# Kernel optimization log

Hardware: AMD Instinct MI355X
Metric: run time of the kernel (lower is better)

Reference implementation:

```python
import jax, jax.numpy as jnp
import numpy as np

D_MODEL = 1024
NUM_HEADS = 16
D_K = D_MODEL // NUM_HEADS
B, N = 4, 2048


def setup_inputs() -> dict:
    key = jax.random.key(0)
    ks = jax.random.split(key, 5)
    scale = 1.0 / np.sqrt(D_MODEL)
    return {
        "x": jax.random.normal(ks[0], (B, N, D_MODEL), dtype=jnp.float32),
        "wq": jax.random.normal(ks[1], (D_MODEL, D_MODEL), dtype=jnp.float32) * scale,
        "wk": jax.random.normal(ks[2], (D_MODEL, D_MODEL), dtype=jnp.float32) * scale,
        "wv": jax.random.normal(ks[3], (D_MODEL, D_MODEL), dtype=jnp.float32) * scale,
        "wo": jax.random.normal(ks[4], (D_MODEL, D_MODEL), dtype=jnp.float32) * scale,
    }


def reference(x, wq, wk, wv, wo):
    b, n, d = x.shape
    # torch Linear(weight W) computes x @ W.T
    def proj(w):
        return (x @ w.T).reshape(b, n, NUM_HEADS, D_K).transpose(0, 2, 1, 3)  # [B,H,N,d_k]
    Q, K, V = proj(wq), proj(wk), proj(wv)
    scores = jnp.einsum("bhqd,bhkd->bhqk", Q, K) / jnp.sqrt(jnp.float32(D_K))
    causal = jnp.tril(jnp.ones((n, n), dtype=bool))
    scores = jnp.where(causal, scores, jnp.float32(-jnp.inf))
    attn = jax.nn.softmax(scores, axis=-1)
    vals = jnp.einsum("bhqk,bhkd->bhqd", attn, V)  # [B,H,N,d_k]
    vals = vals.transpose(0, 2, 1, 3).reshape(b, n, d)
    out = vals @ wo.T
    return (out, K, V)
```

## Files before the change

### kernel.cpp

```cpp
#include <hip/hip_runtime.h>
#include <hip/hip_bf16.h>

typedef __bf16 bf16_t;
typedef __bf16 bf16x8 __attribute__((ext_vector_type(8)));
typedef __bf16 bf16x4 __attribute__((ext_vector_type(4)));
typedef float f32x4 __attribute__((ext_vector_type(4)));
typedef float f32x16 __attribute__((ext_vector_type(16)));
typedef int i32x4 __attribute__((ext_vector_type(4)));

#define LDS_AS __attribute__((address_space(3)))
#define GLB_AS __attribute__((address_space(1)))

__device__ __forceinline__ void gload_lds16(const void* g, void* l) {
  __builtin_amdgcn_global_load_lds((const GLB_AS void*)g, (LDS_AS void*)l, 16, 0, 0);
}

static __device__ __forceinline__ f32x4 mfma16(bf16x8 a, bf16x8 b, f32x4 c) {
  return __builtin_amdgcn_mfma_f32_16x16x32_bf16(a, b, c, 0, 0, 0);
}
static __device__ __forceinline__ f32x16 mfma32(bf16x8 a, bf16x8 b, f32x16 c) {
  return __builtin_amdgcn_mfma_f32_32x32x16_bf16(a, b, c, 0, 0, 0);
}
__device__ __forceinline__ int cvtpk_bf16(float lo, float hi) {
  int r;
  asm("v_cvt_pk_bf16_f32 %0, %1, %2" : "=v"(r) : "v"(lo), "v"(hi));
  return r;
}
__device__ __forceinline__ bf16x8 mkfrag(int w0, int w1, int w2, int w3) {
  i32x4 v;
  v[0] = w0; v[1] = w1; v[2] = w2; v[3] = w3;
  return __builtin_bit_cast(bf16x8, v);
}

#define PIPE_TILE_END()                                        \
  asm volatile("s_waitcnt vmcnt(0)" ::: "memory");             \
  __builtin_amdgcn_s_barrier();                                \
  asm volatile("" ::: "memory");                               \
  __builtin_amdgcn_sched_barrier(0)

__device__ __forceinline__ void xcd_rc(int orig, int& rowI, int& colI) {
  int logical = ((orig & 7) << 6) | (orig >> 3);
  rowI = logical >> 3;
  colI = logical & 7;
}

#define QSCALE 0.18033688011112042f

__global__ __launch_bounds__(256) void cast_kernel(
    const float* __restrict__ x, const float* __restrict__ wq,
    const float* __restrict__ wk, const float* __restrict__ wv,
    const float* __restrict__ wo, bf16_t* __restrict__ xb,
    bf16_t* __restrict__ wqb, bf16_t* __restrict__ wkb,
    bf16_t* __restrict__ wvb, bf16_t* __restrict__ wob) {
  size_t i = ((size_t)blockIdx.x * 256 + threadIdx.x) * 4;
  const float* s;
  bf16_t* d;
  size_t off;
  if (i < 8388608) {
    s = x; d = xb; off = i;
  } else {
    size_t j = i - 8388608;
    int wi = (int)(j >> 20);
    off = j & 1048575;
    s = wi == 0 ? wq : wi == 1 ? wk : wi == 2 ? wv : wo;
    d = wi == 0 ? wqb : wi == 1 ? wkb : wi == 2 ? wvb : wob;
  }
  float4 v = *(const float4*)(s + off);
  bf16x4 o;
  o[0] = (bf16_t)v.x; o[1] = (bf16_t)v.y; o[2] = (bf16_t)v.z; o[3] = (bf16_t)v.w;
  *(bf16x4*)(d + off) = o;
}

__global__ __launch_bounds__(512) void gemm_qkv(
    const bf16_t* __restrict__ xb, const bf16_t* __restrict__ wqb,
    const bf16_t* __restrict__ wkb, const bf16_t* __restrict__ wvb,
    bf16_t* __restrict__ Qb, bf16_t* __restrict__ Kb, bf16_t* __restrict__ vTb,
    float* __restrict__ outK, float* __restrict__ outV) {
  __shared__ __align__(16) bf16_t lds[32768];
  const int tid = threadIdx.x;
  const int lane = tid & 63, w = tid >> 6;
  const int llo = lane & 15, lhi = lane >> 4;
  const int wm = w >> 2, wn = w & 3;
  int rowI, colI;
  xcd_rc(blockIdx.x, rowI, colI);
  const int rowBase = rowI * 128, colW = colI * 128;

  const int arow = tid >> 2, asrc = (tid & 3) ^ ((arow >> 1) & 3);
  const bf16_t* srcA = xb + (size_t)(rowBase + arow) * 1024 + asrc * 8;
  const bf16_t* srcB0 = wqb + (size_t)(colW + arow) * 1024 + asrc * 8;
  const bf16_t* srcB1 = wkb + (size_t)(colW + arow) * 1024 + asrc * 8;
  const bf16_t* srcB2 = wvb + (size_t)(colW + arow) * 1024 + asrc * 8;
  const int dstA = tid * 8;
  const int dstB0 = 4096 + tid * 8;
  const int dstB1 = 4096 + (512 + tid) * 8;
  const int dstB2 = 4096 + (1024 + tid) * 8;

  auto STAGE = [&](int kt, int b) {
    bf16_t* base = lds + b * 16384;
    gload_lds16(srcA + kt * 32, base + dstA);
    gload_lds16(srcB0 + kt * 32, base + dstB0);
    gload_lds16(srcB1 + kt * 32, base + dstB1);
    gload_lds16(srcB2 + kt * 32, base + dstB2);
  };

  f32x4 acc[4][6] = {};
  const int xr = (llo >> 1) & 3;
  STAGE(0, 0);
  PIPE_TILE_END();
  for (int kt = 0; kt < 32; ++kt) {
    if (kt + 1 < 32) STAGE(kt + 1, (kt + 1) & 1);
    __builtin_amdgcn_sched_barrier(0);
    const bf16_t* bufA = lds + (kt & 1) * 16384;
    const bf16_t* bufB = bufA + 4096;
    bf16x8 aF[4], bF[6];
#pragma unroll
    for (int mf = 0; mf < 4; ++mf)
      aF[mf] = *(const bf16x8*)&bufA[(wm * 64 + mf * 16 + llo) * 32 +
                                     ((lhi ^ xr) * 8)];
#pragma unroll
    for (int nf = 0; nf < 6; ++nf)
      bF[nf] = *(const bf16x8*)&bufB[(wn * 96 + nf * 16 + llo) * 32 +
                                     ((lhi ^ xr) * 8)];
    __builtin_amdgcn_s_setprio(1);
#pragma unroll
    for (int mf = 0; mf < 4; ++mf)
#pragma unroll
      for (int nf = 0; nf < 6; ++nf) acc[mf][nf] = mfma16(aF[mf], bF[nf], acc[mf][nf]);
    __builtin_amdgcn_s_setprio(0);
    PIPE_TILE_END();
  }

#pragma unroll
  for (int mf = 0; mf < 4; ++mf) {
    int m0 = rowBase + wm * 64 + mf * 16 + lhi * 4;
    int b = m0 >> 11, tok0 = m0 & 2047;
#pragma unroll
    for (int nf = 0; nf < 6; ++nf) {
      int n = wn * 96 + nf * 16 + llo;
      int mat = n >> 7;
      int nm = colW + (n & 127);
      int h = nm >> 6, dk = nm & 63;
      size_t hoff = ((size_t)(b * 16 + h) * 2048 + tok0) * 64 + dk;
      if (mat == 0) {
#pragma unroll
        for (int r = 0; r < 4; ++r)
          Qb[hoff + (size_t)r * 64] = (bf16_t)(acc[mf][nf][r] * QSCALE);
      } else if (mat == 1) {
#pragma unroll
        for (int r = 0; r < 4; ++r) {
          outK[hoff + (size_t)r * 64] = acc[mf][nf][r];
          Kb[hoff + (size_t)r * 64] = (bf16_t)acc[mf][nf][r];
        }
      } else {
#pragma unroll
        for (int r = 0; r < 4; ++r) outV[hoff + (size_t)r * 64] = acc[mf][nf][r];
        bf16x4 pk;
#pragma unroll
        for (int r = 0; r < 4; ++r) pk[r] = (bf16_t)acc[mf][nf][r];
        *(bf16x4*)&vTb[((size_t)(b * 16 + h) * 64 + dk) * 2048 + tok0] = pk;
      }
    }
  }
}

__global__ __launch_bounds__(256) void gemm_out(const bf16_t* __restrict__ valsb,
                                                const bf16_t* __restrict__ wob,
                                                float* __restrict__ out) {
  __shared__ __align__(16) bf16_t lds[16384];
  const int tid = threadIdx.x;
  const int lane = tid & 63, w = tid >> 6;
  const int llo = lane & 15, lhi = lane >> 4;
  const int wm = w >> 1, wn = w & 1;
  int rowI, colI;
  xcd_rc(blockIdx.x, rowI, colI);
  const int rowBase = rowI * 128, colW = colI * 128;

  int g0 = tid, g1 = 256 + tid;
  int r0 = g0 >> 2, r1 = g1 >> 2;
  int s0 = (g0 & 3) ^ ((r0 >> 1) & 3), s1 = (g1 & 3) ^ ((r1 >> 1) & 3);
  const bf16_t* srcA0 = valsb + (size_t)(rowBase + r0) * 1024 + s0 * 8;
  const bf16_t* srcA1 = valsb + (size_t)(rowBase + r1) * 1024 + s1 * 8;
  const bf16_t* srcB0 = wob + (size_t)(colW + r0) * 1024 + s0 * 8;
  const bf16_t* srcB1 = wob + (size_t)(colW + r1) * 1024 + s1 * 8;
  const int dA0 = g0 * 8, dA1 = g1 * 8;
  const int dB0 = 4096 + g0 * 8, dB1 = 4096 + g1 * 8;

  auto STAGE = [&](int kt, int b) {
    bf16_t* base = lds + b * 8192;
    gload_lds16(srcA0 + kt * 32, base + dA0);
    gload_lds16(srcA1 + kt * 32, base + dA1);
    gload_lds16(srcB0 + kt * 32, base + dB0);
    gload_lds16(srcB1 + kt * 32, base + dB1);
  };

  f32x4 acc[4][4] = {};
  const int xr = (llo >> 1) & 3;
  STAGE(0, 0);
  PIPE_TILE_END();
  for (int kt = 0; kt < 32; ++kt) {
    if (kt + 1 < 32) STAGE(kt + 1, (kt + 1) & 1);
    __builtin_amdgcn_sched_barrier(0);
    const bf16_t* bufA = lds + (kt & 1) * 8192;
    const bf16_t* bufB = bufA + 4096;
    bf16x8 aF[4], bF[4];
#pragma unroll
    for (int mf = 0; mf < 4; ++mf)
      aF[mf] = *(const bf16x8*)&bufA[(wm * 64 + mf * 16 + llo) * 32 +
                                     ((lhi ^ xr) * 8)];
#pragma unroll
    for (int nf = 0; nf < 4; ++nf)
      bF[nf] = *(const bf16x8*)&bufB[(wn * 64 + nf * 16 + llo) * 32 +
                                     ((lhi ^ xr) * 8)];
    __builtin_amdgcn_s_setprio(1);
#pragma unroll
    for (int mf = 0; mf < 4; ++mf)
#pragma unroll
      for (int nf = 0; nf < 4; ++nf) acc[mf][nf] = mfma16(aF[mf], bF[nf], acc[mf][nf]);
    __builtin_amdgcn_s_setprio(0);
    PIPE_TILE_END();
  }
#pragma unroll
  for (int mf = 0; mf < 4; ++mf) {
    int m0 = rowBase + wm * 64 + mf * 16 + lhi * 4;
#pragma unroll
    for (int nf = 0; nf < 4; ++nf) {
      int n = colW + wn * 64 + nf * 16 + llo;
#pragma unroll
      for (int r = 0; r < 4; ++r) out[(size_t)(m0 + r) * 1024 + n] = acc[mf][nf][r];
    }
  }
}

__global__ __launch_bounds__(256, 3) void attn_kernel(
    const bf16_t* __restrict__ Qb, const bf16_t* __restrict__ Kb,
    const bf16_t* __restrict__ vTb, bf16_t* __restrict__ valsb) {
  __shared__ bf16_t kS[2][64 * 64];
  __shared__ bf16_t vS[2][64 * 64];
  const int tid = threadIdx.x;
  const int w = tid >> 6, lane = tid & 63;
  const int ql = lane & 31, hi = lane >> 5, hi4 = hi * 4;
  const int head = blockIdx.x;
  const int qseg = 15 - blockIdx.y;
  const int qbase = qseg * 128;
  const int qw = qbase + w * 32;
  const int qrow = qw + ql;
  const int nkt = qseg * 2 + 2;
  const bf16_t* Qh = Qb + (size_t)head * 131072;
  const bf16_t* Kh = Kb + (size_t)head * 131072;
  const bf16_t* Vh = vTb + (size_t)head * 131072;

  bf16x8 qB[4];
#pragma unroll
  for (int kk = 0; kk < 4; ++kk)
    qB[kk] = *(const bf16x8*)&Qh[(size_t)qrow * 64 + kk * 16 + hi * 8];

  i32x4 ov;
  ov[0] = ov[1] = ov[2] = ov[3] = 0x3F803F80;
  const bf16x8 onesF = __builtin_bit_cast(bf16x8, ov);

  f32x16 oacc0 = {}, oacc1 = {};
  f32x16 lacc = {};

  const int c0 = tid, c1 = 256 + tid;
  const int r0 = c0 >> 3, r1 = c1 >> 3;
  const int s0 = (c0 & 7) ^ ((r0 ^ (r0 >> 3)) & 7);
  const int s1 = (c1 & 7) ^ ((r1 ^ (r1 >> 3)) & 7);

  auto STAGE = [&](int kt_, int bi) {
    const int kb_ = kt_ * 64;
    gload_lds16(Kh + (size_t)(kb_ + r0) * 64 + s0 * 8, &kS[bi][c0 * 8]);
    gload_lds16(Kh + (size_t)(kb_ + r1) * 64 + s1 * 8, &kS[bi][c1 * 8]);
    gload_lds16(Vh + (size_t)r0 * 2048 + kb_ + s0 * 8, &vS[bi][c0 * 8]);
    gload_lds16(Vh + (size_t)r1 * 2048 + kb_ + s1 * 8, &vS[bi][c1 * 8]);
  };

  const int swzA = (ql ^ (ql >> 3)) & 7;
  const int swzB = swzA ^ 4;

  STAGE(0, 0);
  __syncthreads();
  int cur = 0;
  for (int kt = 0; kt < nkt; ++kt) {
    const int kbase = kt * 64;
    if (kt + 1 < nkt) STAGE(kt + 1, cur ^ 1);
    if (kbase <= qw) {
      const bf16_t* kb = kS[cur];
      const bf16_t* vb = vS[cur];
      f32x16 st0 = {}, st1 = {};
      __builtin_amdgcn_s_setprio(1);
#pragma unroll
      for (int kk = 0; kk < 4; ++kk) {
        bf16x8 kf0 = *(const bf16x8*)&kb[ql * 64 + (((kk * 2 + hi) ^ swzA) * 8)];
        st0 = mfma32(kf0, qB[kk], st0);
      }
#pragma unroll
      for (int kk = 0; kk < 4; ++kk) {
        bf16x8 kf1 = *(const bf16x8*)&kb[(32 + ql) * 64 + (((kk * 2 + hi) ^ swzB) * 8)];
        st1 = mfma32(kf1, qB[kk], st1);
      }
      __builtin_amdgcn_s_setprio(0);
      if (kbase + 64 > qw) {
        const int lim = qrow - kbase;
#pragma unroll
        for (int rg = 0; rg < 16; ++rg) {
          const int kof = (rg & 3) + 8 * (rg >> 2) + hi4;
          if (kof > lim) st0[rg] = -__builtin_inff();
          if (kof + 32 > lim) st1[rg] = -__builtin_inff();
        }
      }
#pragma unroll
      for (int j = 0; j < 16; ++j) {
        st0[j] = __builtin_amdgcn_exp2f(st0[j]);
        st1[j] = __builtin_amdgcn_exp2f(st1[j]);
      }
      int a0 = cvtpk_bf16(st0[0], st0[1]), a1 = cvtpk_bf16(st0[2], st0[3]);
      int a2 = cvtpk_bf16(st0[4], st0[5]), a3 = cvtpk_bf16(st0[6], st0[7]);
      int a4 = cvtpk_bf16(st0[8], st0[9]), a5 = cvtpk_bf16(st0[10], st0[11]);
      int a6 = cvtpk_bf16(st0[12], st0[13]), a7 = cvtpk_bf16(st0[14], st0[15]);
      int b0 = cvtpk_bf16(st1[0], st1[1]), b1 = cvtpk_bf16(st1[2], st1[3]);
      int b2 = cvtpk_bf16(st1[4], st1[5]), b3 = cvtpk_bf16(st1[6], st1[7]);
      int b4 = cvtpk_bf16(st1[8], st1[9]), b5 = cvtpk_bf16(st1[10], st1[11]);
      int b6 = cvtpk_bf16(st1[12], st1[13]), b7 = cvtpk_bf16(st1[14], st1[15]);
      auto s02 = __builtin_amdgcn_permlane32_swap(a0, a2, false, false);
      auto s13 = __builtin_amdgcn_permlane32_swap(a1, a3, false, false);
      auto s46 = __builtin_amdgcn_permlane32_swap(a4, a6, false, false);
      auto s57 = __builtin_amdgcn_permlane32_swap(a5, a7, false, false);
      auto t02 = __builtin_amdgcn_permlane32_swap(b0, b2, false, false);
      auto t13 = __builtin_amdgcn_permlane32_swap(b1, b3, false, false);
      auto t46 = __builtin_amdgcn_permlane32_swap(b4, b6, false, false);
      auto t57 = __builtin_amdgcn_permlane32_swap(b5, b7, false, false);
      bf16x8 pB0 = mkfrag(s02[0], s13[0], s02[1], s13[1]);
      bf16x8 pB1 = mkfrag(s46[0], s57[0], s46[1], s57[1]);
      bf16x8 pB2 = mkfrag(t02[0], t13[0], t02[1], t13[1]);
      bf16x8 pB3 = mkfrag(t46[0], t57[0], t46[1], t57[1]);
      __builtin_amdgcn_s_setprio(1);
#pragma unroll
      for (int ks = 0; ks < 4; ++ks) {
        bf16x8 pb = ks == 0 ? pB0 : ks == 1 ? pB1 : ks == 2 ? pB2 : pB3;
        bf16x8 vf0 = *(const bf16x8*)&vb[ql * 64 + (((ks * 2 + hi) ^ swzA) * 8)];
        oacc0 = mfma32(vf0, pb, oacc0);
        bf16x8 vf1 = *(const bf16x8*)&vb[(32 + ql) * 64 + (((ks * 2 + hi) ^ swzB) * 8)];
        oacc1 = mfma32(vf1, pb, oacc1);
        lacc = mfma32(onesF, pb, lacc);
      }
      __builtin_amdgcn_s_setprio(0);
    }
    __syncthreads();
    cur ^= 1;
  }
  const float inv = 1.f / lacc[0];
  size_t base = ((size_t)(head >> 4) * 2048 + qrow) * 1024 + (head & 15) * 64 + hi4;
#pragma unroll
  for (int rg = 0; rg < 4; ++rg) {
    bf16x4 o0, o1;
#pragma unroll
    for (int j = 0; j < 4; ++j) {
      o0[j] = (bf16_t)(oacc0[rg * 4 + j] * inv);
      o1[j] = (bf16_t)(oacc1[rg * 4 + j] * inv);
    }
    *(bf16x4*)&valsb[base + rg * 8] = o0;
    *(bf16x4*)&valsb[base + 32 + rg * 8] = o1;
  }
}

extern "C" void kernel_launch(void* const* d_in, const int* in_sizes, int n_in,
                              void* d_out, int out_size, void* d_ws, size_t ws_size,
                              hipStream_t stream) {
  const float* x = (const float*)d_in[0];
  const float* wq = (const float*)d_in[1];
  const float* wk = (const float*)d_in[2];
  const float* wv = (const float*)d_in[3];
  const float* wo = (const float*)d_in[4];
  float* out = (float*)d_out;
  float* outK = out + 8388608;
  float* outV = out + 16777216;
  bf16_t* xb = (bf16_t*)d_ws;
  bf16_t* wqb = xb + 8388608;
  bf16_t* wkb = wqb + 1048576;
  bf16_t* wvb = wkb + 1048576;
  bf16_t* wob = wvb + 1048576;
  bf16_t* Qb = wob + 1048576;
  bf16_t* Kb = Qb + 8388608;
  bf16_t* vTb = Kb + 8388608;
  bf16_t* valsb = vTb + 8388608;
  cast_kernel<<<12288, 256, 0, stream>>>(x, wq, wk, wv, wo, xb, wqb, wkb, wvb, wob);
  gemm_qkv<<<512, 512, 0, stream>>>(xb, wqb, wkb, wvb, Qb, Kb, vTb, outK, outV);
  attn_kernel<<<dim3(64, 16), 256, 0, stream>>>(Qb, Kb, vTb, valsb);
  gemm_out<<<512, 256, 0, stream>>>(valsb, wob, out);
}
```

Measured before the change: 160.3 us.

## Rewrite QKV GEMM with 256x256 tiles, K=64 steps, and phased load pipeline

The QKV projection now uses 256x256 output tiles per block, each covering a single weight matrix, with K-steps of 64 and 128KB of dynamic LDS. Global-to-LDS loads are spread across four compute phases per K-tile, with fine-grained vmcnt/lgkmcnt waits and barriers, and an 8-way XOR swizzle replaces the old 4-way one. The goal is more reuse per loaded byte and more overlap of loads with MFMA work. In exchange the grid drops to 384 blocks, each with a large register and LDS footprint, which lowers occupancy and may leave some CUs idle.

```diff
diff --git a/kernel.cpp b/kernel.cpp
--- a/kernel.cpp
+++ b/kernel.cpp
@@ -37,12 +37,6 @@
   __builtin_amdgcn_s_barrier();                                \
   asm volatile("" ::: "memory");                               \
   __builtin_amdgcn_sched_barrier(0)
-
-__device__ __forceinline__ void xcd_rc(int orig, int& rowI, int& colI) {
-  int logical = ((orig & 7) << 6) | (orig >> 3);
-  rowI = logical >> 3;
-  colI = logical & 7;
-}
 
 #define QSCALE 0.18033688011112042f
 
@@ -71,74 +65,115 @@
   *(bf16x4*)(d + off) = o;
 }
 
-__global__ __launch_bounds__(512) void gemm_qkv(
+#define PHASE(qq, bA, bB, RDB, STAGES, VMW)                                      \
+  do {                                                                           \
+    if (RDB) {                                                                   \
+      _Pragma("unroll") for (int nf = 0; nf < 4; ++nf)                           \
+          _Pragma("unroll") for (int ks = 0; ks < 2; ++ks)                       \
+              bF[nf * 2 + ks] = ldfrag(bB, wn * 64 + nf * 16 + llo, ks);         \
+    }                                                                            \
+    _Pragma("unroll") for (int m2 = 0; m2 < 2; ++m2)                             \
+        _Pragma("unroll") for (int ks = 0; ks < 2; ++ks)                         \
+            aF[m2 * 2 + ks] = ldfrag(bA, wm * 128 + (qq * 2 + m2) * 16 + llo, ks);\
+    STAGES;                                                                      \
+    if (RDB) asm volatile("s_waitcnt lgkmcnt(8)" ::: "memory");                  \
+    __builtin_amdgcn_s_barrier();                                                \
+    asm volatile("s_waitcnt lgkmcnt(0)" ::: "memory");                           \
+    __builtin_amdgcn_sched_barrier(0);                                           \
+    __builtin_amdgcn_s_setprio(1);                                               \
+    _Pragma("unroll") for (int m2 = 0; m2 < 2; ++m2)                             \
+        _Pragma("unroll") for (int nf = 0; nf < 4; ++nf)                         \
+            _Pragma("unroll") for (int ks = 0; ks < 2; ++ks)                     \
+                acc[qq * 2 + m2][nf] =                                           \
+                    mfma16(aF[m2 * 2 + ks], bF[nf * 2 + ks], acc[qq * 2 + m2][nf]);\
+    __builtin_amdgcn_s_setprio(0);                                               \
+    VMW;                                                                         \
+    __builtin_amdgcn_s_barrier();                                                \
+    asm volatile("" ::: "memory");                                               \
+  } while (0)
+
+__global__ __launch_bounds__(512, 2) void gemm_qkv(
     const bf16_t* __restrict__ xb, const bf16_t* __restrict__ wqb,
     const bf16_t* __restrict__ wkb, const bf16_t* __restrict__ wvb,
     bf16_t* __restrict__ Qb, bf16_t* __restrict__ Kb, bf16_t* __restrict__ vTb,
     float* __restrict__ outK, float* __restrict__ outV) {
-  __shared__ __align__(16) bf16_t lds[32768];
+  extern __shared__ __align__(16) bf16_t lds[];
   const int tid = threadIdx.x;
   const int lane = tid & 63, w = tid >> 6;
   const int llo = lane & 15, lhi = lane >> 4;
   const int wm = w >> 2, wn = w & 3;
-  int rowI, colI;
-  xcd_rc(blockIdx.x, rowI, colI);
-  const int rowBase = rowI * 128, colW = colI * 128;
-
-  const int arow = tid >> 2, asrc = (tid & 3) ^ ((arow >> 1) & 3);
-  const bf16_t* srcA = xb + (size_t)(rowBase + arow) * 1024 + asrc * 8;
-  const bf16_t* srcB0 = wqb + (size_t)(colW + arow) * 1024 + asrc * 8;
-  const bf16_t* srcB1 = wkb + (size_t)(colW + arow) * 1024 + asrc * 8;
-  const bf16_t* srcB2 = wvb + (size_t)(colW + arow) * 1024 + asrc * 8;
-  const int dstA = tid * 8;
-  const int dstB0 = 4096 + tid * 8;
-  const int dstB1 = 4096 + (512 + tid) * 8;
-  const int dstB2 = 4096 + (1024 + tid) * 8;
-
-  auto STAGE = [&](int kt, int b) {
-    bf16_t* base = lds + b * 16384;
-    gload_lds16(srcA + kt * 32, base + dstA);
-    gload_lds16(srcB0 + kt * 32, base + dstB0);
-    gload_lds16(srcB1 + kt * 32, base + dstB1);
-    gload_lds16(srcB2 + kt * 32, base + dstB2);
+  const int orig = blockIdx.x;
+  const int logical = (orig & 7) * 48 + (orig >> 3);
+  const int rowI = logical / 12, colI = logical % 12;
+  const int rowBase = rowI * 256;
+  const int mat = colI >> 2;
+  const int colInMat = (colI & 3) * 256;
+  const bf16_t* Wsrc = mat == 0 ? wqb : (mat == 1 ? wkb : wvb);
+
+  const int r0 = tid >> 3;
+  const int sc = (tid & 7) ^ ((r0 ^ (r0 >> 3)) & 7);
+  const bf16_t* aSrcBase = xb + (size_t)(rowBase + r0) * 1024 + sc * 8;
+  const bf16_t* bSrcBase = Wsrc + (size_t)(colInMat + r0) * 1024 + sc * 8;
+
+  auto SA = [&](int kt, int s, int j) {
+    gload_lds16(aSrcBase + (size_t)j * 65536 + kt * 64,
+                lds + s * 16384 + (j * 512 + tid) * 8);
   };
-
-  f32x4 acc[4][6] = {};
-  const int xr = (llo >> 1) & 3;
-  STAGE(0, 0);
-  PIPE_TILE_END();
-  for (int kt = 0; kt < 32; ++kt) {
-    if (kt + 1 < 32) STAGE(kt + 1, (kt + 1) & 1);
-    __builtin_amdgcn_sched_barrier(0);
-    const bf16_t* bufA = lds + (kt & 1) * 16384;
-    const bf16_t* bufB = bufA + 4096;
-    bf16x8 aF[4], bF[6];
-#pragma unroll
-    for (int mf = 0; mf < 4; ++mf)
-      aF[mf] = *(const bf16x8*)&bufA[(wm * 64 + mf * 16 + llo) * 32 +
-                                     ((lhi ^ xr) * 8)];
-#pragma unroll
-    for (int nf = 0; nf < 6; ++nf)
-      bF[nf] = *(const bf16x8*)&bufB[(wn * 96 + nf * 16 + llo) * 32 +
-                                     ((lhi ^ xr) * 8)];
-    __builtin_amdgcn_s_setprio(1);
-#pragma unroll
-    for (int mf = 0; mf < 4; ++mf)
-#pragma unroll
-      for (int nf = 0; nf < 6; ++nf) acc[mf][nf] = mfma16(aF[mf], bF[nf], acc[mf][nf]);
-    __builtin_amdgcn_s_setprio(0);
-    PIPE_TILE_END();
-  }
-
-#pragma unroll
-  for (int mf = 0; mf < 4; ++mf) {
-    int m0 = rowBase + wm * 64 + mf * 16 + lhi * 4;
+  auto SB = [&](int kt, int s, int j) {
+    gload_lds16(bSrcBase + (size_t)j * 65536 + kt * 64,
+                lds + 32768 + s * 16384 + (j * 512 + tid) * 8);
+  };
+  auto ldfrag = [&](const bf16_t* buf, int row, int ks) {
+    int sw = (row ^ (row >> 3)) & 7;
+    return *(const bf16x8*)&buf[row * 64 + (((ks * 4 + lhi) ^ sw) * 8)];
+  };
+
+  f32x4 acc[8][4] = {};
+  bf16x8 bF[8], aF[4];
+
+  const bf16_t* A0 = lds;
+  const bf16_t* A1 = lds + 16384;
+  const bf16_t* B0 = lds + 32768;
+  const bf16_t* B1 = lds + 49152;
+
+  SA(0, 0, 0); SA(0, 0, 1); SA(0, 0, 2); SA(0, 0, 3);
+  SB(0, 0, 0); SB(0, 0, 1); SB(0, 0, 2); SB(0, 0, 3);
+  SB(1, 1, 0); SB(1, 1, 1); SB(1, 1, 2); SB(1, 1, 3);
+  SA(1, 1, 0); SA(1, 1, 2);
+  asm volatile("s_waitcnt vmcnt(6)" ::: "memory");
+  __builtin_amdgcn_s_barrier();
+  asm volatile("" ::: "memory");
+
+  for (int it = 0; it < 8; ++it) {
+    const int kt0 = 2 * it, kt1 = kt0 + 1;
+    const bool nl = it < 7;
+    PHASE(0, A0, B0, true, { SA(kt1, 1, 1); SA(kt1, 1, 3); }, {});
+    PHASE(1, A0, B0, false,
+          { if (nl) { SB(kt0 + 2, 0, 0); SB(kt0 + 2, 0, 1); } }, {});
+    PHASE(2, A0, B0, false,
+          { if (nl) { SB(kt0 + 2, 0, 2); SB(kt0 + 2, 0, 3); } }, {});
+    PHASE(3, A0, B0, false,
+          { if (nl) { SA(kt0 + 2, 0, 0); SA(kt0 + 2, 0, 2); } },
+          { if (nl) asm volatile("s_waitcnt vmcnt(6)" ::: "memory");
+            else    asm volatile("s_waitcnt vmcnt(0)" ::: "memory"); });
+    PHASE(0, A1, B1, true,
+          { if (nl) { SA(kt0 + 2, 0, 1); SA(kt0 + 2, 0, 3); } }, {});
+    PHASE(1, A1, B1, false,
+          { if (nl) { SB(kt1 + 2, 1, 0); SB(kt1 + 2, 1, 1); } }, {});
+    PHASE(2, A1, B1, false,
+          { if (nl) { SB(kt1 + 2, 1, 2); SB(kt1 + 2, 1, 3); } }, {});
+    PHASE(3, A1, B1, false,
+          { if (nl) { SA(kt1 + 2, 1, 0); SA(kt1 + 2, 1, 2); } },
+          { if (nl) asm volatile("s_waitcnt vmcnt(6)" ::: "memory"); });
+  }
+
+#pragma unroll
+  for (int mf = 0; mf < 8; ++mf) {
+    int m0 = rowBase + wm * 128 + mf * 16 + lhi * 4;
     int b = m0 >> 11, tok0 = m0 & 2047;
 #pragma unroll
-    for (int nf = 0; nf < 6; ++nf) {
-      int n = wn * 96 + nf * 16 + llo;
-      int mat = n >> 7;
-      int nm = colW + (n & 127);
+    for (int nf = 0; nf < 4; ++nf) {
+      int nm = colInMat + wn * 64 + nf * 16 + llo;
       int h = nm >> 6, dk = nm & 63;
       size_t hoff = ((size_t)(b * 16 + h) * 2048 + tok0) * 64 + dk;
       if (mat == 0) {
@@ -163,10 +198,16 @@
   }
 }
 
+__device__ __forceinline__ void xcd_rc(int orig, int& rowI, int& colI) {
+  int logical = ((orig & 7) << 6) | (orig >> 3);
+  rowI = logical >> 3;
+  colI = logical & 7;
+}
+
 __global__ __launch_bounds__(256) void gemm_out(const bf16_t* __restrict__ valsb,
                                                 const bf16_t* __restrict__ wob,
                                                 float* __restrict__ out) {
-  __shared__ __align__(16) bf16_t lds[16384];
+  __shared__ __align__(16) bf16_t slds[16384];
   const int tid = threadIdx.x;
   const int lane = tid & 63, w = tid >> 6;
   const int llo = lane & 15, lhi = lane >> 4;
@@ -186,7 +227,7 @@
   const int dB0 = 4096 + g0 * 8, dB1 = 4096 + g1 * 8;
 
   auto STAGE = [&](int kt, int b) {
-    bf16_t* base = lds + b * 8192;
+    bf16_t* base = slds + b * 8192;
     gload_lds16(srcA0 + kt * 32, base + dA0);
     gload_lds16(srcA1 + kt * 32, base + dA1);
     gload_lds16(srcB0 + kt * 32, base + dB0);
@@ -200,7 +241,7 @@
   for (int kt = 0; kt < 32; ++kt) {
     if (kt + 1 < 32) STAGE(kt + 1, (kt + 1) & 1);
     __builtin_amdgcn_sched_barrier(0);
-    const bf16_t* bufA = lds + (kt & 1) * 8192;
+    const bf16_t* bufA = slds + (kt & 1) * 8192;
     const bf16_t* bufB = bufA + 4096;
     bf16x8 aF[4], bF[4];
 #pragma unroll
@@ -384,7 +425,7 @@
   bf16_t* vTb = Kb + 8388608;
   bf16_t* valsb = vTb + 8388608;
   cast_kernel<<<12288, 256, 0, stream>>>(x, wq, wk, wv, wo, xb, wqb, wkb, wvb, wob);
-  gemm_qkv<<<512, 512, 0, stream>>>(xb, wqb, wkb, wvb, Qb, Kb, vTb, outK, outV);
+  gemm_qkv<<<384, 512, 131072, stream>>>(xb, wqb, wkb, wvb, Qb, Kb, vTb, outK, outV);
   attn_kernel<<<dim3(64, 16), 256, 0, stream>>>(Qb, Kb, vTb, valsb);
   gemm_out<<<512, 256, 0, stream>>>(valsb, wob, out);
 }
```

After: 168.9 us. 1.05x slower.

## Split GEMM k-loop into two phases interleaving LDS reads, prefetch and MFMA

Applied to the files above, without the earlier changes.

Restructures the QKV and output-projection GEMM main loops into two phases per k-tile. Each phase reads half of the B fragments from LDS, issues part of the next tile's global-to-LDS prefetch, and runs half the MFMAs, with barriers around each phase. The goal is to spread memory traffic across the MFMA work and keep waves in lockstep so loads overlap compute better. In exchange it doubles the number of barriers per iteration and adds extra lgkmcnt waits.

```diff
diff --git a/kernel.cpp b/kernel.cpp
--- a/kernel.cpp
+++ b/kernel.cpp
@@ -32,11 +32,15 @@
   return __builtin_bit_cast(bf16x8, v);
 }
 
-#define PIPE_TILE_END()                                        \
-  asm volatile("s_waitcnt vmcnt(0)" ::: "memory");             \
+#define PH_ENTER()                                             \
+  __builtin_amdgcn_sched_barrier(0);                           \
   __builtin_amdgcn_s_barrier();                                \
-  asm volatile("" ::: "memory");                               \
+  asm volatile("s_waitcnt lgkmcnt(0)" ::: "memory");           \
   __builtin_amdgcn_sched_barrier(0)
+
+#define PH_EXIT()                                              \
+  __builtin_amdgcn_sched_barrier(0);                           \
+  __builtin_amdgcn_s_barrier()
 
 __device__ __forceinline__ void xcd_rc(int orig, int& rowI, int& colI) {
   int logical = ((orig & 7) << 6) | (orig >> 3);
@@ -95,39 +99,65 @@
   const int dstB1 = 4096 + (512 + tid) * 8;
   const int dstB2 = 4096 + (1024 + tid) * 8;
 
-  auto STAGE = [&](int kt, int b) {
-    bf16_t* base = lds + b * 16384;
-    gload_lds16(srcA + kt * 32, base + dstA);
-    gload_lds16(srcB0 + kt * 32, base + dstB0);
-    gload_lds16(srcB1 + kt * 32, base + dstB1);
-    gload_lds16(srcB2 + kt * 32, base + dstB2);
+  auto SA = [&](int kt, int b) {
+    gload_lds16(srcA + kt * 32, lds + b * 16384 + dstA);
+  };
+  auto SB0 = [&](int kt, int b) {
+    gload_lds16(srcB0 + kt * 32, lds + b * 16384 + dstB0);
+  };
+  auto SB1 = [&](int kt, int b) {
+    gload_lds16(srcB1 + kt * 32, lds + b * 16384 + dstB1);
+  };
+  auto SB2 = [&](int kt, int b) {
+    gload_lds16(srcB2 + kt * 32, lds + b * 16384 + dstB2);
   };
 
   f32x4 acc[4][6] = {};
   const int xr = (llo >> 1) & 3;
-  STAGE(0, 0);
-  PIPE_TILE_END();
+  SA(0, 0); SB0(0, 0); SB1(0, 0); SB2(0, 0);
+  asm volatile("s_waitcnt vmcnt(0)" ::: "memory");
+  __builtin_amdgcn_s_barrier();
+  asm volatile("" ::: "memory");
+
   for (int kt = 0; kt < 32; ++kt) {
-    if (kt + 1 < 32) STAGE(kt + 1, (kt + 1) & 1);
-    __builtin_amdgcn_sched_barrier(0);
     const bf16_t* bufA = lds + (kt & 1) * 16384;
     const bf16_t* bufB = bufA + 4096;
+    const bool nl = kt + 1 < 32;
+    const int nb = (kt + 1) & 1;
     bf16x8 aF[4], bF[6];
 #pragma unroll
     for (int mf = 0; mf < 4; ++mf)
       aF[mf] = *(const bf16x8*)&bufA[(wm * 64 + mf * 16 + llo) * 32 +
                                      ((lhi ^ xr) * 8)];
 #pragma unroll
-    for (int nf = 0; nf < 6; ++nf)
+    for (int nf = 0; nf < 3; ++nf)
       bF[nf] = *(const bf16x8*)&bufB[(wn * 96 + nf * 16 + llo) * 32 +
                                      ((lhi ^ xr) * 8)];
+    if (nl) { SA(kt + 1, nb); SB0(kt + 1, nb); }
+    PH_ENTER();
     __builtin_amdgcn_s_setprio(1);
 #pragma unroll
     for (int mf = 0; mf < 4; ++mf)
 #pragma unroll
-      for (int nf = 0; nf < 6; ++nf) acc[mf][nf] = mfma16(aF[mf], bF[nf], acc[mf][nf]);
+      for (int nf = 0; nf < 3; ++nf)
+        acc[mf][nf] = mfma16(aF[mf], bF[nf], acc[mf][nf]);
     __builtin_amdgcn_s_setprio(0);
-    PIPE_TILE_END();
+    PH_EXIT();
+#pragma unroll
+    for (int nf = 3; nf < 6; ++nf)
+      bF[nf] = *(const bf16x8*)&bufB[(wn * 96 + nf * 16 + llo) * 32 +
+                                     ((lhi ^ xr) * 8)];
+    if (nl) { SB1(kt + 1, nb); SB2(kt + 1, nb); }
+    PH_ENTER();
+    __builtin_amdgcn_s_setprio(1);
+#pragma unroll
+    for (int mf = 0; mf < 4; ++mf)
+#pragma unroll
+      for (int nf = 3; nf < 6; ++nf)
+        acc[mf][nf] = mfma16(aF[mf], bF[nf], acc[mf][nf]);
+    __builtin_amdgcn_s_setprio(0);
+    asm volatile("s_waitcnt vmcnt(0)" ::: "memory");
+    PH_EXIT();
   }
 
 #pragma unroll
@@ -166,7 +196,7 @@
 __global__ __launch_bounds__(256) void gemm_out(const bf16_t* __restrict__ valsb,
                                                 const bf16_t* __restrict__ wob,
                                                 float* __restrict__ out) {
-  __shared__ __align__(16) bf16_t lds[16384];
+  __shared__ __align__(16) bf16_t slds[16384];
   const int tid = threadIdx.x;
   const int lane = tid & 63, w = tid >> 6;
   const int llo = lane & 15, lhi = lane >> 4;
@@ -185,39 +215,61 @@
   const int dA0 = g0 * 8, dA1 = g1 * 8;
   const int dB0 = 4096 + g0 * 8, dB1 = 4096 + g1 * 8;
 
-  auto STAGE = [&](int kt, int b) {
-    bf16_t* base = lds + b * 8192;
-    gload_lds16(srcA0 + kt * 32, base + dA0);
-    gload_lds16(srcA1 + kt * 32, base + dA1);
-    gload_lds16(srcB0 + kt * 32, base + dB0);
-    gload_lds16(srcB1 + kt * 32, base + dB1);
+  auto SA = [&](int kt, int b) {
+    gload_lds16(srcA0 + kt * 32, slds + b * 8192 + dA0);
+    gload_lds16(srcA1 + kt * 32, slds + b * 8192 + dA1);
+  };
+  auto SB = [&](int kt, int b) {
+    gload_lds16(srcB0 + kt * 32, slds + b * 8192 + dB0);
+    gload_lds16(srcB1 + kt * 32, slds + b * 8192 + dB1);
   };
 
   f32x4 acc[4][4] = {};
   const int xr = (llo >> 1) & 3;
-  STAGE(0, 0);
-  PIPE_TILE_END();
+  SA(0, 0); SB(0, 0);
+  asm volatile("s_waitcnt vmcnt(0)" ::: "memory");
+  __builtin_amdgcn_s_barrier();
+  asm volatile("" ::: "memory");
+
   for (int kt = 0; kt < 32; ++kt) {
-    if (kt + 1 < 32) STAGE(kt + 1, (kt + 1) & 1);
-    __builtin_amdgcn_sched_barrier(0);
-    const bf16_t* bufA = lds + (kt & 1) * 8192;
+    const bf16_t* bufA = slds + (kt & 1) * 8192;
     const bf16_t* bufB = bufA + 4096;
+    const bool nl = kt + 1 < 32;
+    const int nb = (kt + 1) & 1;
     bf16x8 aF[4], bF[4];
 #pragma unroll
     for (int mf = 0; mf < 4; ++mf)
       aF[mf] = *(const bf16x8*)&bufA[(wm * 64 + mf * 16 + llo) * 32 +
                                      ((lhi ^ xr) * 8)];
 #pragma unroll
-    for (int nf = 0; nf < 4; ++nf)
+    for (int nf = 0; nf < 2; ++nf)
       bF[nf] = *(const bf16x8*)&bufB[(wn * 64 + nf * 16 + llo) * 32 +
                                      ((lhi ^ xr) * 8)];
+    if (nl) SA(kt + 1, nb);
+    PH_ENTER();
     __builtin_amdgcn_s_setprio(1);
 #pragma unroll
     for (int mf = 0; mf < 4; ++mf)
 #pragma unroll
-      for (int nf = 0; nf < 4; ++nf) acc[mf][nf] = mfma16(aF[mf], bF[nf], acc[mf][nf]);
+      for (int nf = 0; nf < 2; ++nf)
+        acc[mf][nf] = mfma16(aF[mf], bF[nf], acc[mf][nf]);
     __builtin_amdgcn_s_setprio(0);
-    PIPE_TILE_END();
+    PH_EXIT();
+#pragma unroll
+    for (int nf = 2; nf < 4; ++nf)
+      bF[nf] = *(const bf16x8*)&bufB[(wn * 64 + nf * 16 + llo) * 32 +
+                                     ((lhi ^ xr) * 8)];
+    if (nl) SB(kt + 1, nb);
+    PH_ENTER();
+    __builtin_amdgcn_s_setprio(1);
+#pragma unroll
+    for (int mf = 0; mf < 4; ++mf)
+#pragma unroll
+      for (int nf = 2; nf < 4; ++nf)
+        acc[mf][nf] = mfma16(aF[mf], bF[nf], acc[mf][nf]);
+    __builtin_amdgcn_s_setprio(0);
+    asm volatile("s_waitcnt vmcnt(0)" ::: "memory");
+    PH_EXIT();
   }
 #pragma unroll
   for (int mf = 0; mf < 4; ++mf) {
```

Result: slower. 171.3 us (+6.9%).

## Triple-buffer QKV GEMM LDS pipeline with explicit vmcnt waits

Applied to the files above, without the earlier changes.

Moves the QKV projection GEMM from a double-buffered to a triple-buffered LDS pipeline in dynamic shared memory (96 KB). Loads are issued three K-tiles ahead, with explicit vmcnt waits and barriers before and after compute. The goal is to hide global-load latency better. In exchange it uses more LDS and adds a barrier per iteration, and the occupancy hint of 2 blocks per CU may not be reachable with 96 KB of LDS per block.

```diff
diff --git a/kernel.cpp b/kernel.cpp
--- a/kernel.cpp
+++ b/kernel.cpp
@@ -71,12 +71,12 @@
   *(bf16x4*)(d + off) = o;
 }
 
-__global__ __launch_bounds__(512) void gemm_qkv(
+__global__ __launch_bounds__(512, 2) void gemm_qkv(
     const bf16_t* __restrict__ xb, const bf16_t* __restrict__ wqb,
     const bf16_t* __restrict__ wkb, const bf16_t* __restrict__ wvb,
     bf16_t* __restrict__ Qb, bf16_t* __restrict__ Kb, bf16_t* __restrict__ vTb,
     float* __restrict__ outK, float* __restrict__ outV) {
-  __shared__ __align__(16) bf16_t lds[32768];
+  extern __shared__ __align__(16) bf16_t lds[];
   const int tid = threadIdx.x;
   const int lane = tid & 63, w = tid >> 6;
   const int llo = lane & 15, lhi = lane >> 4;
@@ -106,11 +106,22 @@
   f32x4 acc[4][6] = {};
   const int xr = (llo >> 1) & 3;
   STAGE(0, 0);
-  PIPE_TILE_END();
+  STAGE(1, 1);
+  STAGE(2, 2);
+
+  int cur = 0;
   for (int kt = 0; kt < 32; ++kt) {
-    if (kt + 1 < 32) STAGE(kt + 1, (kt + 1) & 1);
+    if (kt < 30)
+      asm volatile("s_waitcnt vmcnt(8)" ::: "memory");
+    else if (kt == 30)
+      asm volatile("s_waitcnt vmcnt(4)" ::: "memory");
+    else
+      asm volatile("s_waitcnt vmcnt(0)" ::: "memory");
+    __builtin_amdgcn_s_barrier();
+    asm volatile("" ::: "memory");
     __builtin_amdgcn_sched_barrier(0);
-    const bf16_t* bufA = lds + (kt & 1) * 16384;
+
+    const bf16_t* bufA = lds + cur * 16384;
     const bf16_t* bufB = bufA + 4096;
     bf16x8 aF[4], bF[6];
 #pragma unroll
@@ -127,7 +138,13 @@
 #pragma unroll
       for (int nf = 0; nf < 6; ++nf) acc[mf][nf] = mfma16(aF[mf], bF[nf], acc[mf][nf]);
     __builtin_amdgcn_s_setprio(0);
-    PIPE_TILE_END();
+
+    __builtin_amdgcn_sched_barrier(0);
+    __builtin_amdgcn_s_barrier();
+    asm volatile("" ::: "memory");
+    __builtin_amdgcn_sched_barrier(0);
+    if (kt + 3 < 32) STAGE(kt + 3, cur);
+    cur = cur == 2 ? 0 : cur + 1;
   }
 
 #pragma unroll
@@ -166,7 +183,7 @@
 __global__ __launch_bounds__(256) void gemm_out(const bf16_t* __restrict__ valsb,
                                                 const bf16_t* __restrict__ wob,
                                                 float* __restrict__ out) {
-  __shared__ __align__(16) bf16_t lds[16384];
+  __shared__ __align__(16) bf16_t slds[16384];
   const int tid = threadIdx.x;
   const int lane = tid & 63, w = tid >> 6;
   const int llo = lane & 15, lhi = lane >> 4;
@@ -186,7 +203,7 @@
   const int dB0 = 4096 + g0 * 8, dB1 = 4096 + g1 * 8;
 
   auto STAGE = [&](int kt, int b) {
-    bf16_t* base = lds + b * 8192;
+    bf16_t* base = slds + b * 8192;
     gload_lds16(srcA0 + kt * 32, base + dA0);
     gload_lds16(srcA1 + kt * 32, base + dA1);
     gload_lds16(srcB0 + kt * 32, base + dB0);
@@ -200,7 +217,7 @@
   for (int kt = 0; kt < 32; ++kt) {
     if (kt + 1 < 32) STAGE(kt + 1, (kt + 1) & 1);
     __builtin_amdgcn_sched_barrier(0);
-    const bf16_t* bufA = lds + (kt & 1) * 8192;
+    const bf16_t* bufA = slds + (kt & 1) * 8192;
     const bf16_t* bufB = bufA + 4096;
     bf16x8 aF[4], bF[4];
 #pragma unroll
@@ -384,7 +401,7 @@
   bf16_t* vTb = Kb + 8388608;
   bf16_t* valsb = vTb + 8388608;
   cast_kernel<<<12288, 256, 0, stream>>>(x, wq, wk, wv, wo, xb, wqb, wkb, wvb, wob);
-  gemm_qkv<<<512, 512, 0, stream>>>(xb, wqb, wkb, wvb, Qb, Kb, vTb, outK, outV);
+  gemm_qkv<<<512, 512, 98304, stream>>>(xb, wqb, wkb, wvb, Qb, Kb, vTb, outK, outV);
   attn_kernel<<<dim3(64, 16), 256, 0, stream>>>(Qb, Kb, vTb, valsb);
   gemm_out<<<512, 256, 0, stream>>>(valsb, wob, out);
 }
```

New measurement: 161.1 us. About the same (+0.5%).
